# Kernel optimization log

Hardware: AMD Instinct MI355X
Metric: run time of the kernel (lower is better)

## Reference

```python
import jax, jax.numpy as jnp
import numpy as np

WIN = 9  # window size per spatial dim (default [9,9,9] for 3D)


def _window_sum(x):
    # Depthwise conv with an all-ones [9,9,9] kernel, stride 1, zero pad 4
    # == sliding-window box sum. lax.reduce_window is the efficient, exact form.
    pad = WIN // 2
    return jax.lax.reduce_window(
        x, 0.0, jax.lax.add,
        window_dimensions=(1, 1, WIN, WIN, WIN),
        window_strides=(1, 1, 1, 1, 1),
        padding=((0, 0), (0, 0), (pad, pad), (pad, pad), (pad, pad)),
    )


def setup_inputs() -> dict:
    key = jax.random.key(0)
    k1, k2 = jax.random.split(key)
    shape = (2, 1, 160, 160, 160)  # [B, C, D, H, W]
    y_true = jax.random.normal(k1, shape, dtype=jnp.float32)
    y_pred = jax.random.normal(k2, shape, dtype=jnp.float32)
    return {"y_true": y_true, "y_pred": y_pred}


def reference(y_true, y_pred):
    Ii, Ji = y_true, y_pred
    win_size = jnp.asarray(WIN ** 3, dtype=Ii.dtype)  # 729

    I2 = Ii * Ii
    J2 = Ji * Ji
    IJ = Ii * Ji

    I_sum = _window_sum(Ii)
    J_sum = _window_sum(Ji)
    I2_sum = _window_sum(I2)
    J2_sum = _window_sum(J2)
    IJ_sum = _window_sum(IJ)

    u_I = I_sum / win_size
    u_J = J_sum / win_size

    cross = IJ_sum - u_J * I_sum - u_I * J_sum + u_I * u_J * win_size
    I_var = I2_sum - 2.0 * u_I * I_sum + u_I * u_I * win_size
    J_var = J2_sum - 2.0 * u_J * J_sum + u_J * u_J * win_size

    cc = cross * cross / (I_var * J_var + 1e-05)
    # mean over spatial dims [2,3,4] -> [B,C], then mean -> scalar
    return (1.0 - jnp.mean(cc, axis=(2, 3, 4))).mean()
```

## Files before the change

kernel.cpp:

```cpp
#include <hip/hip_runtime.h>


typedef float floatx2 __attribute__((ext_vector_type(2)));

constexpr int W = 160, H = 160, D = 160;
constexpr int SLICE = W * H;
constexpr int NVOX  = W * H * D;
constexpr int BATCH = 2;
constexpr int FROW  = 5 * W;
constexpr float RW  = 1.0f / 729.0f;

constexpr int TPB_ZX = 320;
constexpr int ROWS_PB = 8;
constexpr int XGZ   = W / 4;
constexpr int CHZ   = 5, NCHZ = D / CHZ;
constexpr int NTUP_ZX = BATCH * NCHZ * H;
constexpr int NBLK_ZX = NTUP_ZX / ROWS_PB;
constexpr int LROW  = 168;

constexpr int TPB_Y = 256;
constexpr int XGY   = W / 8;
constexpr int CHY   = 2, NCHY = H / CHY;
constexpr int NTH_Y = BATCH * D * NCHY * XGY;
constexpr int NBLK_Y = NTH_Y / TPB_Y;

__device__ inline unsigned int pk4(float a, float b, float c, float d) {
    unsigned int u = 0;
    u = __builtin_amdgcn_cvt_pk_fp8_f32(a, b, u, false);
    u = __builtin_amdgcn_cvt_pk_fp8_f32(c, d, u, true);
    return u;
}
__device__ inline void up8(uint2 v, float* o) {
    floatx2 t;
    t = __builtin_amdgcn_cvt_pk_f32_fp8(v.x, false); o[0] = t[0]; o[1] = t[1];
    t = __builtin_amdgcn_cvt_pk_f32_fp8(v.x, true);  o[2] = t[0]; o[3] = t[1];
    t = __builtin_amdgcn_cvt_pk_f32_fp8(v.y, false); o[4] = t[0]; o[5] = t[1];
    t = __builtin_amdgcn_cvt_pk_f32_fp8(v.y, true);  o[6] = t[0]; o[7] = t[1];
}

__global__ __launch_bounds__(TPB_ZX) void pass_zx(const float* __restrict__ I,
                                                  const float* __restrict__ J,
                                                  unsigned char* __restrict__ outA) {
    __shared__ float lds[ROWS_PB][5][LROW];

    int tid = threadIdx.x;
    int r  = tid / XGZ;
    int xg = tid % XGZ;
    int tuple = blockIdx.x * ROWS_PB + r;
    int y = tuple % H;
    int c = (tuple / H) % NCHZ;
    int b = tuple / (H * NCHZ);
    int x0 = xg * 4;
    const float* Ib = I + (size_t)b * NVOX + y * W + x0;
    const float* Jb = J + (size_t)b * NVOX + y * W + x0;
    unsigned char* ob = outA + ((size_t)b * D * H + y) * FROW + x0;

    if (xg == 0) {
#pragma unroll
        for (int f = 0; f < 5; ++f) {
            lds[r][f][0] = 0.f; lds[r][f][1] = 0.f;
            lds[r][f][2] = 0.f; lds[r][f][3] = 0.f;
        }
    }
    if (xg == XGZ - 1) {
#pragma unroll
        for (int f = 0; f < 5; ++f) {
            lds[r][f][164] = 0.f; lds[r][f][165] = 0.f;
            lds[r][f][166] = 0.f; lds[r][f][167] = 0.f;
        }
    }

    float s[5][4];
#pragma unroll
    for (int f = 0; f < 5; ++f)
#pragma unroll
        for (int i = 0; i < 4; ++i) s[f][i] = 0.f;

    auto addS = [&](int zz) {
        float4 a = *(const float4*)(Ib + (size_t)zz * SLICE);
        float4 bb = *(const float4*)(Jb + (size_t)zz * SLICE);
        float av[4] = {a.x, a.y, a.z, a.w};
        float bv[4] = {bb.x, bb.y, bb.z, bb.w};
#pragma unroll
        for (int i = 0; i < 4; ++i) {
            float x = av[i], yv = bv[i];
            s[0][i] += x; s[1][i] += yv;
            s[2][i] += x * x; s[3][i] += yv * yv; s[4][i] += x * yv;
        }
    };

    int z0 = c * CHZ;
    for (int zz = (z0 - 4 < 0 ? 0 : z0 - 4); zz <= z0 + 4; ++zz) addS(zz);

    for (int dz = 0; dz < CHZ; ++dz) {
        int z = z0 + dz;
        int za = z + 5, zs = z - 4;
        bool ha = za < D, hs = zs >= 0;
        float4 Az = ha ? *(const float4*)(Ib + (size_t)za * SLICE) : make_float4(0.f, 0.f, 0.f, 0.f);
        float4 Bz = ha ? *(const float4*)(Jb + (size_t)za * SLICE) : make_float4(0.f, 0.f, 0.f, 0.f);
        float4 As = hs ? *(const float4*)(Ib + (size_t)zs * SLICE) : make_float4(0.f, 0.f, 0.f, 0.f);
        float4 Bs = hs ? *(const float4*)(Jb + (size_t)zs * SLICE) : make_float4(0.f, 0.f, 0.f, 0.f);

#pragma unroll
        for (int f = 0; f < 5; ++f)
            *(float4*)&lds[r][f][4 + x0] = make_float4(s[f][0], s[f][1], s[f][2], s[f][3]);
        __syncthreads();

        unsigned char* op = ob + (size_t)z * (H * FROW);
#pragma unroll
        for (int f = 0; f < 5; ++f) {
            float4 Lv = *(const float4*)&lds[r][f][x0];
            float4 Rv = *(const float4*)&lds[r][f][x0 + 8];
            float p0 = Lv.x;
            float p1 = p0 + Lv.y;
            float p2 = p1 + Lv.z;
            float p3 = p2 + Lv.w;
            float p4 = p3 + s[f][0];
            float p5 = p4 + s[f][1];
            float p6 = p5 + s[f][2];
            float p7 = p6 + s[f][3];
            float p8 = p7 + Rv.x;
            float p9 = p8 + Rv.y;
            float p10 = p9 + Rv.z;
            float p11 = p10 + Rv.w;
            *(unsigned int*)(op + f * W) = pk4(p8, p9 - p0, p10 - p1, p11 - p2);
        }
        __syncthreads();

        float ae[4] = {Az.x, Az.y, Az.z, Az.w};
        float be[4] = {Bz.x, Bz.y, Bz.z, Bz.w};
        float al[4] = {As.x, As.y, As.z, As.w};
        float bl[4] = {Bs.x, Bs.y, Bs.z, Bs.w};
#pragma unroll
        for (int i = 0; i < 4; ++i) {
            s[0][i] += ae[i] - al[i];
            s[1][i] += be[i] - bl[i];
            s[2][i] += ae[i] * ae[i] - al[i] * al[i];
            s[3][i] += be[i] * be[i] - bl[i] * bl[i];
            s[4][i] += ae[i] * be[i] - al[i] * bl[i];
        }
    }
}

__global__ __launch_bounds__(TPB_Y) void pass_y(const unsigned char* __restrict__ A,
                                                double* __restrict__ partials) {
    int tid = threadIdx.x;
    int t = blockIdx.x * TPB_Y + tid;
    int xg = t % XGY;
    int tup = t / XGY;
    int yc = tup % NCHY;
    int z  = (tup / NCHY) % D;
    int b  = tup / (NCHY * D);
    int x0 = xg * 8;
    const unsigned char* __restrict__ base =
        A + (size_t)(b * D + z) * H * FROW + x0;
    int y0 = yc * CHY;

    float s[5][8];
#pragma unroll
    for (int f = 0; f < 5; ++f)
#pragma unroll
        for (int i = 0; i < 8; ++i) s[f][i] = 0.f;

    int ylo = y0 - 4 < 0 ? 0 : y0 - 4;
    int yhi = y0 + 4 > H - 1 ? H - 1 : y0 + 4;
    for (int yy = ylo; yy <= yhi; ++yy) {
        const unsigned char* rp = base + (size_t)yy * FROW;
#pragma unroll
        for (int f = 0; f < 5; ++f) {
            uint2 v = *(const uint2*)(rp + f * W);
            float u[8]; up8(v, u);
#pragma unroll
            for (int i = 0; i < 8; ++i) s[f][i] += u[i];
        }
    }

    double acc = 0.0;
#pragma unroll
    for (int dy = 0; dy < CHY; ++dy) {
        int ye = y0 + dy + 5, yl = y0 + dy - 4;
        bool he = ye < H, hl = yl >= 0;
        uint2 pe[5], pl[5];
        const unsigned char* pre = base + (size_t)(he ? ye : 0) * FROW;
        const unsigned char* prl = base + (size_t)(hl ? yl : 0) * FROW;
#pragma unroll
        for (int f = 0; f < 5; ++f) {
            pe[f] = he ? *(const uint2*)(pre + f * W) : make_uint2(0u, 0u);
            pl[f] = hl ? *(const uint2*)(prl + f * W) : make_uint2(0u, 0u);
        }

        float rowcc = 0.f;
#pragma unroll
        for (int i = 0; i < 8; ++i) {
            float Is = s[0][i], Js = s[1][i];
            float I2s = s[2][i], J2s = s[3][i], IJs = s[4][i];
            float tI = RW * Is;
            float cross = __builtin_fmaf(-tI, Js, IJs);
            float Iv    = __builtin_fmaf(-tI, Is, I2s);
            float Jv    = __builtin_fmaf(-(RW * Js), Js, J2s);
            float den   = __builtin_fmaf(Iv, Jv, 1e-5f);
            rowcc = __builtin_fmaf(cross * cross, __builtin_amdgcn_rcpf(den), rowcc);
        }
        acc += (double)rowcc;

#pragma unroll
        for (int f = 0; f < 5; ++f) {
            float ue[8], ul[8];
            up8(pe[f], ue); up8(pl[f], ul);
#pragma unroll
            for (int i = 0; i < 8; ++i) s[f][i] += ue[i] - ul[i];
        }
    }

#pragma unroll
    for (int off = 32; off > 0; off >>= 1) acc += __shfl_down(acc, off);
    __shared__ double sm[TPB_Y / 64];
    if ((tid & 63) == 0) sm[tid >> 6] = acc;
    __syncthreads();
    if (tid == 0) {
        double tt = 0.0;
#pragma unroll
        for (int i = 0; i < TPB_Y / 64; ++i) tt += sm[i];
        partials[blockIdx.x] = tt;
    }
}

__global__ __launch_bounds__(256) void finalize(const double* __restrict__ p,
                                                float* __restrict__ out) {
    double v = 0.0;
    for (int i = threadIdx.x; i < NBLK_Y; i += 256) v += p[i];
#pragma unroll
    for (int off = 32; off > 0; off >>= 1) v += __shfl_down(v, off);
    __shared__ double sm[4];
    int lane = threadIdx.x & 63, wid = threadIdx.x >> 6;
    if (lane == 0) sm[wid] = v;
    __syncthreads();
    if (threadIdx.x == 0) {
        double tt = 0.0;
#pragma unroll
        for (int i = 0; i < 4; ++i) tt += sm[i];
        out[0] = (float)(1.0 - tt / (double)((double)BATCH * (double)NVOX));
    }
}

extern "C" void kernel_launch(void* const* d_in, const int* in_sizes, int n_in,
                              void* d_out, int out_size, void* d_ws, size_t ws_size,
                              hipStream_t stream) {
    const float* I = (const float*)d_in[0];
    const float* J = (const float*)d_in[1];
    float* out = (float*)d_out;

    size_t bufsz = ((size_t)BATCH * 5 * NVOX + 255) / 256 * 256;
    unsigned char* bufA = (unsigned char*)d_ws;
    double* partials = (double*)(bufA + bufsz);

    pass_zx<<<NBLK_ZX, TPB_ZX, 0, stream>>>(I, J, bufA);
    pass_y<<<NBLK_Y, TPB_Y, 0, stream>>>(bufA, partials);
    finalize<<<1, 256, 0, stream>>>(partials, out);
}
```

Baseline: 63.80 us.

## Restructure z/x pass to tile z-chunks in LDS with bf16 x-window sums

Replaces the per-row running z-sum kernel with a block that loads a 40-slice z-halo tile for an 80-wide x-tile. It computes the 9-wide x-box sums from prefix sums in registers, stores them as bf16 in LDS, then each thread sums 9 z-slices for two output planes. This removes the serial z loop with its two barriers per step and gives many more independent blocks, at the cost of re-reading z halos (8 of every 32 slices) and extra x-halo loads. The bf16 intermediate adds rounding error before the fp8 output, and the 9-term z sum is recomputed rather than slid.

```diff
diff --git a/kernel.cpp b/kernel.cpp
--- a/kernel.cpp
+++ b/kernel.cpp
@@ -10,13 +10,13 @@
 constexpr int FROW  = 5 * W;
 constexpr float RW  = 1.0f / 729.0f;
 
-constexpr int TPB_ZX = 320;
-constexpr int ROWS_PB = 8;
-constexpr int XGZ   = W / 4;
-constexpr int CHZ   = 5, NCHZ = D / CHZ;
-constexpr int NTUP_ZX = BATCH * NCHZ * H;
-constexpr int NBLK_ZX = NTUP_ZX / ROWS_PB;
-constexpr int LROW  = 168;
+constexpr int TPB_P = 320;
+constexpr int XT    = 80;
+constexpr int NXT   = W / XT;
+constexpr int CZ    = 32;
+constexpr int NCZ   = D / CZ;
+constexpr int ZS    = CZ + 8;
+constexpr int NBLK_P = BATCH * H * NXT * NCZ;
 
 constexpr int TPB_Y = 256;
 constexpr int XGY   = W / 8;
@@ -37,109 +37,134 @@
     t = __builtin_amdgcn_cvt_pk_f32_fp8(v.y, false); o[4] = t[0]; o[5] = t[1];
     t = __builtin_amdgcn_cvt_pk_f32_fp8(v.y, true);  o[6] = t[0]; o[7] = t[1];
 }
-
-__global__ __launch_bounds__(TPB_ZX) void pass_zx(const float* __restrict__ I,
+__device__ inline unsigned short f2bf(float f) {
+    unsigned int u = __builtin_bit_cast(unsigned int, f);
+    u += 0x7fffu + ((u >> 16) & 1u);
+    return (unsigned short)(u >> 16);
+}
+__device__ inline unsigned int bfpack2(float lo, float hi) {
+    return (unsigned int)f2bf(lo) | ((unsigned int)f2bf(hi) << 16);
+}
+__device__ inline float bflo(unsigned int u) {
+    return __builtin_bit_cast(float, u << 16);
+}
+__device__ inline float bfhi(unsigned int u) {
+    return __builtin_bit_cast(float, u & 0xffff0000u);
+}
+
+__global__ __launch_bounds__(TPB_P) void pass_pzx(const float* __restrict__ I,
                                                   const float* __restrict__ J,
                                                   unsigned char* __restrict__ outA) {
-    __shared__ float lds[ROWS_PB][5][LROW];
-
-    int tid = threadIdx.x;
-    int r  = tid / XGZ;
-    int xg = tid % XGZ;
-    int tuple = blockIdx.x * ROWS_PB + r;
-    int y = tuple % H;
-    int c = (tuple / H) % NCHZ;
-    int b = tuple / (H * NCHZ);
-    int x0 = xg * 4;
-    const float* Ib = I + (size_t)b * NVOX + y * W + x0;
-    const float* Jb = J + (size_t)b * NVOX + y * W + x0;
-    unsigned char* ob = outA + ((size_t)b * D * H + y) * FROW + x0;
-
-    if (xg == 0) {
-#pragma unroll
-        for (int f = 0; f < 5; ++f) {
-            lds[r][f][0] = 0.f; lds[r][f][1] = 0.f;
-            lds[r][f][2] = 0.f; lds[r][f][3] = 0.f;
-        }
-    }
-    if (xg == XGZ - 1) {
-#pragma unroll
-        for (int f = 0; f < 5; ++f) {
-            lds[r][f][164] = 0.f; lds[r][f][165] = 0.f;
-            lds[r][f][166] = 0.f; lds[r][f][167] = 0.f;
-        }
-    }
-
-    float s[5][4];
-#pragma unroll
-    for (int f = 0; f < 5; ++f)
-#pragma unroll
-        for (int i = 0; i < 4; ++i) s[f][i] = 0.f;
-
-    auto addS = [&](int zz) {
-        float4 a = *(const float4*)(Ib + (size_t)zz * SLICE);
-        float4 bb = *(const float4*)(Jb + (size_t)zz * SLICE);
-        float av[4] = {a.x, a.y, a.z, a.w};
-        float bv[4] = {bb.x, bb.y, bb.z, bb.w};
-#pragma unroll
-        for (int i = 0; i < 4; ++i) {
-            float x = av[i], yv = bv[i];
-            s[0][i] += x; s[1][i] += yv;
-            s[2][i] += x * x; s[3][i] += yv * yv; s[4][i] += x * yv;
-        }
-    };
-
-    int z0 = c * CHZ;
-    for (int zz = (z0 - 4 < 0 ? 0 : z0 - 4); zz <= z0 + 4; ++zz) addS(zz);
-
-    for (int dz = 0; dz < CHZ; ++dz) {
-        int z = z0 + dz;
-        int za = z + 5, zs = z - 4;
-        bool ha = za < D, hs = zs >= 0;
-        float4 Az = ha ? *(const float4*)(Ib + (size_t)za * SLICE) : make_float4(0.f, 0.f, 0.f, 0.f);
-        float4 Bz = ha ? *(const float4*)(Jb + (size_t)za * SLICE) : make_float4(0.f, 0.f, 0.f, 0.f);
-        float4 As = hs ? *(const float4*)(Ib + (size_t)zs * SLICE) : make_float4(0.f, 0.f, 0.f, 0.f);
-        float4 Bs = hs ? *(const float4*)(Jb + (size_t)zs * SLICE) : make_float4(0.f, 0.f, 0.f, 0.f);
-
-#pragma unroll
-        for (int f = 0; f < 5; ++f)
-            *(float4*)&lds[r][f][4 + x0] = make_float4(s[f][0], s[f][1], s[f][2], s[f][3]);
-        __syncthreads();
-
-        unsigned char* op = ob + (size_t)z * (H * FROW);
-#pragma unroll
-        for (int f = 0; f < 5; ++f) {
-            float4 Lv = *(const float4*)&lds[r][f][x0];
-            float4 Rv = *(const float4*)&lds[r][f][x0 + 8];
-            float p0 = Lv.x;
-            float p1 = p0 + Lv.y;
-            float p2 = p1 + Lv.z;
-            float p3 = p2 + Lv.w;
-            float p4 = p3 + s[f][0];
-            float p5 = p4 + s[f][1];
-            float p6 = p5 + s[f][2];
-            float p7 = p6 + s[f][3];
-            float p8 = p7 + Rv.x;
-            float p9 = p8 + Rv.y;
-            float p10 = p9 + Rv.z;
-            float p11 = p10 + Rv.w;
-            *(unsigned int*)(op + f * W) = pk4(p8, p9 - p0, p10 - p1, p11 - p2);
-        }
-        __syncthreads();
-
-        float ae[4] = {Az.x, Az.y, Az.z, Az.w};
-        float be[4] = {Bz.x, Bz.y, Bz.z, Bz.w};
-        float al[4] = {As.x, As.y, As.z, As.w};
-        float bl[4] = {Bs.x, Bs.y, Bs.z, Bs.w};
-#pragma unroll
-        for (int i = 0; i < 4; ++i) {
-            s[0][i] += ae[i] - al[i];
-            s[1][i] += be[i] - bl[i];
-            s[2][i] += ae[i] * ae[i] - al[i] * al[i];
-            s[3][i] += be[i] * be[i] - bl[i] * bl[i];
-            s[4][i] += ae[i] * be[i] - al[i] * bl[i];
-        }
-    }
+    __shared__ unsigned short xw[5][ZS][XT];
+
+    int blk = blockIdx.x;
+    int zc = blk % NCZ;
+    int xt = (blk / NCZ) % NXT;
+    int y  = (blk / (NCZ * NXT)) % H;
+    int b  = blk / (NCZ * NXT * H);
+    int tx0 = xt * XT;
+    int zbase = zc * CZ - 4;
+    const float* Ib = I + (size_t)b * NVOX + y * W;
+    const float* Jb = J + (size_t)b * NVOX + y * W;
+
+    const float4 Z4 = make_float4(0.f, 0.f, 0.f, 0.f);
+    for (int u = threadIdx.x; u < ZS * 10; u += TPB_P) {
+        int zs = u / 10;
+        int xu = u % 10;
+        int gxs = tx0 + xu * 8;
+        int gz = zbase + zs;
+        float a[16], c[16];
+        if (gz >= 0 && gz < D) {
+            const float* ip = Ib + (size_t)gz * SLICE + gxs;
+            const float* jp = Jb + (size_t)gz * SLICE + gxs;
+            float4 A0 = (gxs >= 4)      ? *(const float4*)(ip - 4) : Z4;
+            float4 A1 = *(const float4*)(ip);
+            float4 A2 = *(const float4*)(ip + 4);
+            float4 A3 = (gxs + 11 < W)  ? *(const float4*)(ip + 8) : Z4;
+            float4 C0 = (gxs >= 4)      ? *(const float4*)(jp - 4) : Z4;
+            float4 C1 = *(const float4*)(jp);
+            float4 C2 = *(const float4*)(jp + 4);
+            float4 C3 = (gxs + 11 < W)  ? *(const float4*)(jp + 8) : Z4;
+            float at[16] = {A0.x,A0.y,A0.z,A0.w, A1.x,A1.y,A1.z,A1.w,
+                            A2.x,A2.y,A2.z,A2.w, A3.x,A3.y,A3.z,A3.w};
+            float ct[16] = {C0.x,C0.y,C0.z,C0.w, C1.x,C1.y,C1.z,C1.w,
+                            C2.x,C2.y,C2.z,C2.w, C3.x,C3.y,C3.z,C3.w};
+#pragma unroll
+            for (int k = 0; k < 16; ++k) { a[k] = at[k]; c[k] = ct[k]; }
+        } else {
+#pragma unroll
+            for (int k = 0; k < 16; ++k) { a[k] = 0.f; c[k] = 0.f; }
+        }
+#pragma unroll
+        for (int f = 0; f < 5; ++f) {
+            float v[16];
+#pragma unroll
+            for (int k = 0; k < 16; ++k) {
+                float x = a[k], yv = c[k];
+                v[k] = (f == 0) ? x : (f == 1) ? yv :
+                       (f == 2) ? x * x : (f == 3) ? yv * yv : x * yv;
+            }
+            float P[16];
+            P[0] = v[0];
+#pragma unroll
+            for (int k = 1; k < 16; ++k) P[k] = P[k - 1] + v[k];
+            float w[8];
+            w[0] = P[8];
+#pragma unroll
+            for (int j = 1; j < 8; ++j) w[j] = P[j + 8] - P[j - 1];
+            uint2 pk;
+            pk.x = bfpack2(w[0], w[1]) | 0u;
+            pk.y = bfpack2(w[2], w[3]);
+            uint2 pk2;
+            pk2.x = bfpack2(w[4], w[5]);
+            pk2.y = bfpack2(w[6], w[7]);
+            *(uint2*)&xw[f][zs][xu * 8]     = pk;
+            *(uint2*)&xw[f][zs][xu * 8 + 4] = pk2;
+        }
+    }
+
+    __syncthreads();
+
+    int xg = threadIdx.x % 20;
+    int zl = threadIdx.x / 20;
+    int x0l = xg * 4;
+    int zo0 = zl * 2;
+
+    float acc[5][4];
+#pragma unroll
+    for (int f = 0; f < 5; ++f)
+#pragma unroll
+        for (int i = 0; i < 4; ++i) acc[f][i] = 0.f;
+
+#pragma unroll
+    for (int k = 0; k < 9; ++k) {
+#pragma unroll
+        for (int f = 0; f < 5; ++f) {
+            uint2 v = *(const uint2*)&xw[f][zo0 + k][x0l];
+            acc[f][0] += bflo(v.x); acc[f][1] += bfhi(v.x);
+            acc[f][2] += bflo(v.y); acc[f][3] += bfhi(v.y);
+        }
+    }
+
+    int gz0 = zc * CZ + zo0;
+    unsigned char* op0 = outA + ((size_t)(b * D + gz0) * H + y) * FROW + tx0 + x0l;
+#pragma unroll
+    for (int f = 0; f < 5; ++f)
+        *(unsigned int*)(op0 + f * W) = pk4(acc[f][0], acc[f][1], acc[f][2], acc[f][3]);
+
+#pragma unroll
+    for (int f = 0; f < 5; ++f) {
+        uint2 ve = *(const uint2*)&xw[f][zo0 + 9][x0l];
+        uint2 vl = *(const uint2*)&xw[f][zo0][x0l];
+        acc[f][0] += bflo(ve.x) - bflo(vl.x);
+        acc[f][1] += bfhi(ve.x) - bfhi(vl.x);
+        acc[f][2] += bflo(ve.y) - bflo(vl.y);
+        acc[f][3] += bfhi(ve.y) - bfhi(vl.y);
+    }
+    unsigned char* op1 = op0 + (size_t)H * FROW;
+#pragma unroll
+    for (int f = 0; f < 5; ++f)
+        *(unsigned int*)(op1 + f * W) = pk4(acc[f][0], acc[f][1], acc[f][2], acc[f][3]);
 }
 
 __global__ __launch_bounds__(TPB_Y) void pass_y(const unsigned char* __restrict__ A,
@@ -254,7 +279,7 @@
     unsigned char* bufA = (unsigned char*)d_ws;
     double* partials = (double*)(bufA + bufsz);
 
-    pass_zx<<<NBLK_ZX, TPB_ZX, 0, stream>>>(I, J, bufA);
+    pass_pzx<<<NBLK_P, TPB_P, 0, stream>>>(I, J, bufA);
     pass_y<<<NBLK_Y, TPB_Y, 0, stream>>>(bufA, partials);
     finalize<<<1, 256, 0, stream>>>(partials, out);
 }
```

Measured after the change: 64.99 us. Within noise of the previous version (+1.9%).

## Stage y-window rows in LDS and share them across threads in pass_y

Applied to the files above, without the earlier changes.

Rewrites the y-direction pass so each block stages a 48-row strip (40 output rows plus halo) of the fp8 partial-sum buffer into shared memory, then 400 of its threads each compute two output rows from LDS. This replaces the previous per-thread global reloads of the 9-row window, which re-read each row many times from L2/HBM. It adds an LDS footprint of about 38 KB per block and a block-wide barrier, and leaves 48 of 448 threads idle during compute.

```diff
diff --git a/kernel.cpp b/kernel.cpp
--- a/kernel.cpp
+++ b/kernel.cpp
@@ -18,11 +18,12 @@
 constexpr int NBLK_ZX = NTUP_ZX / ROWS_PB;
 constexpr int LROW  = 168;
 
-constexpr int TPB_Y = 256;
-constexpr int XGY   = W / 8;
-constexpr int CHY   = 2, NCHY = H / CHY;
-constexpr int NTH_Y = BATCH * D * NCHY * XGY;
-constexpr int NBLK_Y = NTH_Y / TPB_Y;
+constexpr int TPB_Y = 448;
+constexpr int YQ    = 40;
+constexpr int NYQ   = H / YQ;
+constexpr int YR    = YQ + 8;
+constexpr int NBLK_Y = BATCH * D * NYQ;
+constexpr int LDW   = YR * FROW / 16;
 
 __device__ inline unsigned int pk4(float a, float b, float c, float d) {
     unsigned int u = 0;
@@ -30,12 +31,13 @@
     u = __builtin_amdgcn_cvt_pk_fp8_f32(c, d, u, true);
     return u;
 }
+__device__ inline void up4(unsigned int v, float* o) {
+    floatx2 t;
+    t = __builtin_amdgcn_cvt_pk_f32_fp8(v, false); o[0] = t[0]; o[1] = t[1];
+    t = __builtin_amdgcn_cvt_pk_f32_fp8(v, true);  o[2] = t[0]; o[3] = t[1];
+}
 __device__ inline void up8(uint2 v, float* o) {
-    floatx2 t;
-    t = __builtin_amdgcn_cvt_pk_f32_fp8(v.x, false); o[0] = t[0]; o[1] = t[1];
-    t = __builtin_amdgcn_cvt_pk_f32_fp8(v.x, true);  o[2] = t[0]; o[3] = t[1];
-    t = __builtin_amdgcn_cvt_pk_f32_fp8(v.y, false); o[4] = t[0]; o[5] = t[1];
-    t = __builtin_amdgcn_cvt_pk_f32_fp8(v.y, true);  o[6] = t[0]; o[7] = t[1];
+    up4(v.x, o); up4(v.y, o + 4);
 }
 
 __global__ __launch_bounds__(TPB_ZX) void pass_zx(const float* __restrict__ I,
@@ -142,79 +144,89 @@
     }
 }
 
-__global__ __launch_bounds__(TPB_Y) void pass_y(const unsigned char* __restrict__ A,
-                                                double* __restrict__ partials) {
+__global__ __launch_bounds__(TPB_Y) void pass_y2(const unsigned char* __restrict__ A,
+                                                 double* __restrict__ partials) {
+    __shared__ unsigned char rows[YR * FROW];
+    __shared__ double sm[TPB_Y / 64];
+
+    int blk = blockIdx.x;
+    int yq = blk % NYQ;
+    int z  = (blk / NYQ) % D;
+    int b  = blk / (NYQ * D);
+    int y0 = yq * YQ;
     int tid = threadIdx.x;
-    int t = blockIdx.x * TPB_Y + tid;
-    int xg = t % XGY;
-    int tup = t / XGY;
-    int yc = tup % NCHY;
-    int z  = (tup / NCHY) % D;
-    int b  = tup / (NCHY * D);
-    int x0 = xg * 8;
-    const unsigned char* __restrict__ base =
-        A + (size_t)(b * D + z) * H * FROW + x0;
-    int y0 = yc * CHY;
-
-    float s[5][8];
-#pragma unroll
-    for (int f = 0; f < 5; ++f)
-#pragma unroll
-        for (int i = 0; i < 8; ++i) s[f][i] = 0.f;
-
-    int ylo = y0 - 4 < 0 ? 0 : y0 - 4;
-    int yhi = y0 + 4 > H - 1 ? H - 1 : y0 + 4;
-    for (int yy = ylo; yy <= yhi; ++yy) {
-        const unsigned char* rp = base + (size_t)yy * FROW;
-#pragma unroll
-        for (int f = 0; f < 5; ++f) {
-            uint2 v = *(const uint2*)(rp + f * W);
-            float u[8]; up8(v, u);
-#pragma unroll
-            for (int i = 0; i < 8; ++i) s[f][i] += u[i];
-        }
-    }
+    const unsigned char* __restrict__ src =
+        A + ((size_t)(b * D + z) * H) * FROW;
+
+    for (int i = tid; i < LDW; i += TPB_Y) {
+        int off = i * 16;
+        int r = off / FROW;
+        int gy = y0 - 4 + r;
+        uint4 v = make_uint4(0u, 0u, 0u, 0u);
+        if (gy >= 0 && gy < H)
+            v = *(const uint4*)(src + (size_t)gy * FROW + (off % FROW));
+        *(uint4*)&rows[off] = v;
+    }
+    __syncthreads();
 
     double acc = 0.0;
-#pragma unroll
-    for (int dy = 0; dy < CHY; ++dy) {
-        int ye = y0 + dy + 5, yl = y0 + dy - 4;
-        bool he = ye < H, hl = yl >= 0;
-        uint2 pe[5], pl[5];
-        const unsigned char* pre = base + (size_t)(he ? ye : 0) * FROW;
-        const unsigned char* prl = base + (size_t)(hl ? yl : 0) * FROW;
-#pragma unroll
-        for (int f = 0; f < 5; ++f) {
-            pe[f] = he ? *(const uint2*)(pre + f * W) : make_uint2(0u, 0u);
-            pl[f] = hl ? *(const uint2*)(prl + f * W) : make_uint2(0u, 0u);
-        }
-
-        float rowcc = 0.f;
-#pragma unroll
-        for (int i = 0; i < 8; ++i) {
-            float Is = s[0][i], Js = s[1][i];
-            float I2s = s[2][i], J2s = s[3][i], IJs = s[4][i];
-            float tI = RW * Is;
-            float cross = __builtin_fmaf(-tI, Js, IJs);
-            float Iv    = __builtin_fmaf(-tI, Is, I2s);
-            float Jv    = __builtin_fmaf(-(RW * Js), Js, J2s);
-            float den   = __builtin_fmaf(Iv, Jv, 1e-5f);
-            rowcc = __builtin_fmaf(cross * cross, __builtin_amdgcn_rcpf(den), rowcc);
-        }
-        acc += (double)rowcc;
-
-#pragma unroll
-        for (int f = 0; f < 5; ++f) {
-            float ue[8], ul[8];
-            up8(pe[f], ue); up8(pl[f], ul);
-#pragma unroll
-            for (int i = 0; i < 8; ++i) s[f][i] += ue[i] - ul[i];
+    if (tid < 400) {
+        int xg = tid % 20;
+        int ys = tid / 20;
+        int rbase = ys * 2;
+        int x8 = xg * 8;
+
+        float s[5][8];
+#pragma unroll
+        for (int f = 0; f < 5; ++f)
+#pragma unroll
+            for (int i = 0; i < 8; ++i) s[f][i] = 0.f;
+
+#pragma unroll
+        for (int t = 0; t < 9; ++t) {
+            const unsigned char* rp = &rows[(rbase + t) * FROW + x8];
+#pragma unroll
+            for (int f = 0; f < 5; ++f) {
+                uint2 v = *(const uint2*)(rp + f * W);
+                float u[8]; up8(v, u);
+#pragma unroll
+                for (int i = 0; i < 8; ++i) s[f][i] += u[i];
+            }
+        }
+
+#pragma unroll
+        for (int o = 0; o < 2; ++o) {
+            float rowcc = 0.f;
+#pragma unroll
+            for (int i = 0; i < 8; ++i) {
+                float Is = s[0][i], Js = s[1][i];
+                float I2s = s[2][i], J2s = s[3][i], IJs = s[4][i];
+                float tI = RW * Is;
+                float cross = __builtin_fmaf(-tI, Js, IJs);
+                float Iv    = __builtin_fmaf(-tI, Is, I2s);
+                float Jv    = __builtin_fmaf(-(RW * Js), Js, J2s);
+                float den   = __builtin_fmaf(Iv, Jv, 1e-5f);
+                rowcc = __builtin_fmaf(cross * cross, __builtin_amdgcn_rcpf(den), rowcc);
+            }
+            acc += (double)rowcc;
+            if (o == 0) {
+                const unsigned char* re = &rows[(rbase + 9) * FROW + x8];
+                const unsigned char* rl = &rows[rbase * FROW + x8];
+#pragma unroll
+                for (int f = 0; f < 5; ++f) {
+                    uint2 ve = *(const uint2*)(re + f * W);
+                    uint2 vl = *(const uint2*)(rl + f * W);
+                    float ue[8], ul[8];
+                    up8(ve, ue); up8(vl, ul);
+#pragma unroll
+                    for (int i = 0; i < 8; ++i) s[f][i] += ue[i] - ul[i];
+                }
+            }
         }
     }
 
 #pragma unroll
     for (int off = 32; off > 0; off >>= 1) acc += __shfl_down(acc, off);
-    __shared__ double sm[TPB_Y / 64];
     if ((tid & 63) == 0) sm[tid >> 6] = acc;
     __syncthreads();
     if (tid == 0) {
@@ -255,6 +267,6 @@
     double* partials = (double*)(bufA + bufsz);
 
     pass_zx<<<NBLK_ZX, TPB_ZX, 0, stream>>>(I, J, bufA);
-    pass_y<<<NBLK_Y, TPB_Y, 0, stream>>>(bufA, partials);
+    pass_y2<<<NBLK_Y, TPB_Y, 0, stream>>>(bufA, partials);
     finalize<<<1, 256, 0, stream>>>(partials, out);
 }
```

New measurement: 64.78 us. No clear change (+1.5%).
